# Kernel tuning notes

Hardware: AMD Instinct MI355X
Metric: run time of the kernel (lower is better)

Reference implementation:

```python
import jax, jax.numpy as jnp
import numpy as np

N_NODES = 100000


def gcn_conv(x, src, dst, W, b, n):
    # PyG GCNConv: h = x @ W; add self-loops; sym-normalize; scatter-add; + bias
    h = x @ W                                        # [N, out]
    loop = jnp.arange(n, dtype=src.dtype)
    src2 = jnp.concatenate([src, loop])              # [E+N]
    dst2 = jnp.concatenate([dst, loop])
    deg = jax.ops.segment_sum(jnp.ones_like(dst2, dtype=h.dtype), dst2, num_segments=n)
    dis = jnp.where(deg > 0, jax.lax.rsqrt(deg), 0.0)
    norm = dis[src2] * dis[dst2]                     # [E+N]
    msg = h[src2] * norm[:, None]                    # gather + scale
    out = jax.ops.segment_sum(msg, dst2, num_segments=n)  # scatter-add
    return out + b


def setup_inputs() -> dict:
    key = jax.random.key(0)
    ks = jax.random.split(key, 8)
    F_in, H = 128, 64
    E = 1200000
    x = jax.random.normal(ks[0], (N_NODES, F_in), dtype=jnp.float32)
    edge_index = jax.random.randint(ks[1], (2, E), 0, N_NODES, dtype=jnp.int64)
    s = 1.0 / np.sqrt(F_in)
    W1 = jax.random.normal(ks[2], (F_in, H), dtype=jnp.float32) * s
    b1 = jnp.zeros((H,), dtype=jnp.float32)
    W2 = jax.random.normal(ks[3], (H, H), dtype=jnp.float32) * (1.0 / np.sqrt(H))
    b2 = jnp.zeros((H,), dtype=jnp.float32)
    W3 = jax.random.normal(ks[4], (H, 1), dtype=jnp.float32) * (1.0 / np.sqrt(H))
    b3 = jnp.zeros((1,), dtype=jnp.float32)
    return {"x": x, "edge_index": edge_index, "W1": W1, "b1": b1,
            "W2": W2, "b2": b2, "W3": W3, "b3": b3}


def reference(x, edge_index, W1, b1, W2, b2, W3, b3):
    n = x.shape[0]
    src, dst = edge_index[0], edge_index[1]
    h = jax.nn.relu(gcn_conv(x, src, dst, W1, b1, n))
    h = jax.nn.relu(gcn_conv(h, src, dst, W2, b2, n))
    return (h @ W3 + b3)[:, 0]  # squeeze(-1) -> [N]
```

## Files before the change

kernel.cpp:

```cpp
#include <hip/hip_runtime.h>

#define NF 64
#define NBKMAX 512
#define CHUNK 4096
#define CAP   4096

typedef __attribute__((ext_vector_type(8))) short bf16x8;
typedef __attribute__((ext_vector_type(4))) float f32x4;

__device__ __forceinline__ unsigned short f2bf(float f) {
    union { float f; unsigned u; } c; c.f = f;
    unsigned u = c.u;
    return (unsigned short)((u + 0x7FFFu + ((u >> 16) & 1u)) >> 16);
}
__device__ __forceinline__ float bf2f1(unsigned short v) {
    union { unsigned u; float f; } c; c.u = ((unsigned)v) << 16;
    return c.f;
}
__device__ __forceinline__ float2 bfp2(unsigned v) {
    union { unsigned u; float f; } lo, hi;
    lo.u = v << 16;
    hi.u = v & 0xffff0000u;
    return make_float2(lo.f, hi.f);
}

__global__ void k_zero(int* __restrict__ p, int m) {
    int i = blockIdx.x * blockDim.x + threadIdx.x;
    if (i < m) p[i] = 0;
}

__global__ __launch_bounds__(256) void k_bscatter2(const int* __restrict__ src,
                                                   const int* __restrict__ dst,
                                                   int* __restrict__ bcnt,
                                                   uint2* __restrict__ pairs, int E, int nbk) {
    __shared__ int hist[NBKMAX];
    __shared__ int base[NBKMAX];
    __shared__ uint2 stage[CHUNK];
    int e0 = blockIdx.x * CHUNK;
    int cnt = E - e0; if (cnt > CHUNK) cnt = CHUNK;
    for (int i = threadIdx.x; i < nbk; i += 256) hist[i] = 0;
    __syncthreads();
    for (int i = threadIdx.x; i < cnt; i += 256) {
        int s = src[e0 + i], d = dst[e0 + i];
        stage[i] = make_uint2((unsigned)s, (unsigned)d);
        atomicAdd(&hist[((unsigned)d) >> 8], 1);
    }
    __syncthreads();
    for (int i = threadIdx.x; i < nbk; i += 256) {
        int c = hist[i];
        base[i] = c ? atomicAdd(&bcnt[i], c) : 0;
        hist[i] = 0;
    }
    __syncthreads();
    for (int i = threadIdx.x; i < cnt; i += 256) {
        uint2 p = stage[i];
        int b = p.y >> 8;
        int off = base[b] + atomicAdd(&hist[b], 1);
        if (off < CAP) pairs[(size_t)b * CAP + off] = p;
    }
}

__global__ __launch_bounds__(256) void k_bsort2(const uint2* __restrict__ pairs,
                                                const int* __restrict__ bcnt,
                                                int* __restrict__ start, int* __restrict__ endp,
                                                int* __restrict__ adj,
                                                float* __restrict__ dis, int n) {
    __shared__ int cnt[256];
    __shared__ int cur[256];
    int b   = blockIdx.x;
    int nb  = b << 8;
    int nn  = n - nb; if (nn > 256) nn = 256;
    int ec  = bcnt[b]; if (ec > CAP) ec = CAP;
    int pbI = b * CAP;
    size_t pb = (size_t)pbI;
    int t = threadIdx.x;
    cnt[t] = 0;
    __syncthreads();
    for (int i = t; i < ec; i += 256)
        atomicAdd(&cnt[pairs[pb + i].y & 255], 1);
    __syncthreads();
    int v = cnt[t];
    __syncthreads();
    for (int off = 1; off < 256; off <<= 1) {
        int u = (t >= off) ? cnt[t - off] : 0;
        __syncthreads();
        cnt[t] += u;
        __syncthreads();
    }
    int exc = cnt[t] - v;
    if (t < nn) {
        start[nb + t] = pbI + exc;
        endp[nb + t]  = pbI + exc + v;
        dis[nb + t]   = rsqrtf((float)(v + 1));
    }
    cur[t] = exc;
    __syncthreads();
    for (int i = t; i < ec; i += 256) {
        uint2 p = pairs[pb + i];
        int off = atomicAdd(&cur[p.y & 255], 1);
        adj[pbI + off] = (int)p.x;
    }
}

__global__ void k_wprep(const float* __restrict__ W, unsigned short* __restrict__ Wt_hi,
                        unsigned short* __restrict__ Wt_lo, int K) {
    int idx = blockIdx.x * 256 + threadIdx.x;
    if (idx >= K * 64) return;
    int k = idx >> 6, col = idx & 63;
    float w = W[idx];
    unsigned short h = f2bf(w);
    unsigned short l = f2bf(w - bf2f1(h));
    Wt_hi[col * K + k] = h;
    Wt_lo[col * K + k] = l;
}

__device__ __forceinline__ void load8f(const float* A, bool ok, size_t off, float* v) {
    if (ok) {
        float4 a = *(const float4*)&A[off];
        float4 b = *(const float4*)&A[off + 4];
        v[0]=a.x; v[1]=a.y; v[2]=a.z; v[3]=a.w;
        v[4]=b.x; v[5]=b.y; v[6]=b.z; v[7]=b.w;
    } else { for (int j = 0; j < 8; ++j) v[j] = 0.f; }
}
__device__ __forceinline__ void load8f(const unsigned short* A, bool ok, size_t off, float* v) {
    if (ok) {
        uint4 u = *(const uint4*)&A[off];
        float2 p0 = bfp2(u.x), p1 = bfp2(u.y), p2 = bfp2(u.z), p3 = bfp2(u.w);
        v[0]=p0.x; v[1]=p0.y; v[2]=p1.x; v[3]=p1.y;
        v[4]=p2.x; v[5]=p2.y; v[6]=p3.x; v[7]=p3.y;
    } else { for (int j = 0; j < 8; ++j) v[j] = 0.f; }
}

template<int K, typename AT>
__global__ __launch_bounds__(256) void k_mgemm(const AT* __restrict__ A,
                                               const unsigned short* __restrict__ Wt_hi_g,
                                               const unsigned short* __restrict__ Wt_lo_g,
                                               const float* __restrict__ bias_in,
                                               const float* __restrict__ dis,
                                               unsigned short* __restrict__ out, int n) {
    constexpr int KS = K / 8;
    constexpr int SM = KS - 1;
    __shared__ unsigned short sAh[64 * 32];
    __shared__ unsigned short sAl[64 * 32];
    __shared__ unsigned short sWh[64 * K];
    __shared__ unsigned short sWl[64 * K];
    const int tid = threadIdx.x;
    const int rb = blockIdx.x * 64;
    const int w  = tid >> 6, l = tid & 63;
    const int lr = l & 15, lg = l >> 4;
    const int srow = tid >> 2, skq = tid & 3;

    for (int idx = tid; idx < 64 * KS; idx += 256) {
        int col = idx / KS, slot = idx % KS;
        int d = col * K + 8 * (slot ^ (col & SM));
        *(uint4*)&sWh[d] = *(const uint4*)&Wt_hi_g[col * K + slot * 8];
        *(uint4*)&sWl[d] = *(const uint4*)&Wt_lo_g[col * K + slot * 8];
    }

    f32x4 acc[4] = {};

    for (int kb = 0; kb < K; kb += 32) {
        __syncthreads();
        {
            int rg = rb + srow;
            float v[8];
            load8f(A, rg < n, (size_t)rg * K + kb + skq * 8, v);
            if (bias_in) {
                #pragma unroll
                for (int j = 0; j < 8; ++j)
                    v[j] = fmaxf(v[j] + bias_in[kb + skq * 8 + j], 0.f);
            }
            unsigned short h8[8], l8[8];
            #pragma unroll
            for (int j = 0; j < 8; ++j) {
                h8[j] = f2bf(v[j]);
                l8[j] = f2bf(v[j] - bf2f1(h8[j]));
            }
            int d = srow * 32 + 8 * (skq ^ (srow & 3));
            *(uint4*)&sAh[d] = *(const uint4*)h8;
            *(uint4*)&sAl[d] = *(const uint4*)l8;
        }
        __syncthreads();

        int arow = w * 16 + lr;
        int aoff = arow * 32 + 8 * (lg ^ (arow & 3));
        const bf16x8 ah = *(const bf16x8*)&sAh[aoff];
        const bf16x8 al = *(const bf16x8*)&sAl[aoff];
        #pragma unroll
        for (int ct = 0; ct < 4; ++ct) {
            int col  = ct * 16 + lr;
            int boff = col * K + 8 * ((kb / 8 + lg) ^ (col & SM));
            const bf16x8 bh = *(const bf16x8*)&sWh[boff];
            const bf16x8 bl = *(const bf16x8*)&sWl[boff];
            acc[ct] = __builtin_amdgcn_mfma_f32_16x16x32_bf16(ah, bh, acc[ct], 0, 0, 0);
            acc[ct] = __builtin_amdgcn_mfma_f32_16x16x32_bf16(ah, bl, acc[ct], 0, 0, 0);
            acc[ct] = __builtin_amdgcn_mfma_f32_16x16x32_bf16(al, bh, acc[ct], 0, 0, 0);
        }
    }

    #pragma unroll
    for (int i = 0; i < 4; ++i) {
        int r = rb + w * 16 + lg * 4 + i;
        if (r < n) {
            float sc = dis[r];
            #pragma unroll
            for (int ct = 0; ct < 4; ++ct)
                out[(size_t)r * NF + ct * 16 + lr] = f2bf(acc[ct][i] * sc);
        }
    }
}

__global__ __launch_bounds__(256) void k_gather(const unsigned short* __restrict__ g,
                                                const int* __restrict__ adj,
                                                const int* __restrict__ start,
                                                const int* __restrict__ endp,
                                                const float* __restrict__ dis,
                                                unsigned short* __restrict__ agg, int n) {
    int node = blockIdx.x * 16 + (threadIdx.x >> 4);
    int fl   = threadIdx.x & 15;
    int gb   = threadIdx.x & 48;
    if (node >= n) return;
    int s = start[node], e = endp[node];
    uint2 v = *(const uint2*)&g[(size_t)node * NF + fl * 4];
    float2 pa = bfp2(v.x), pb = bfp2(v.y);
    float4 acc = make_float4(pa.x, pa.y, pb.x, pb.y);
    for (int base = s; base < e; base += 16) {
        int m = e - base; if (m > 16) m = 16;
        int idx = (fl < m) ? adj[base + fl] : 0;
        for (int j = 0; j < m; ++j) {
            int u = __shfl(idx, gb + j);
            uint2 w = *(const uint2*)&g[(size_t)u * NF + fl * 4];
            float2 q0 = bfp2(w.x), q1 = bfp2(w.y);
            acc.x += q0.x; acc.y += q0.y; acc.z += q1.x; acc.w += q1.y;
        }
    }
    float sc = dis[node];
    ushort4 o;
    o.x = f2bf(acc.x * sc);
    o.y = f2bf(acc.y * sc);
    o.z = f2bf(acc.z * sc);
    o.w = f2bf(acc.w * sc);
    *(ushort4*)&agg[(size_t)node * NF + fl * 4] = o;
}

__global__ __launch_bounds__(256) void k_gather_final(const unsigned short* __restrict__ g,
                                                      const int* __restrict__ adj,
                                                      const int* __restrict__ start,
                                                      const int* __restrict__ endp,
                                                      const float* __restrict__ dis,
                                                      const float* __restrict__ b2,
                                                      const float* __restrict__ W3,
                                                      const float* __restrict__ b3,
                                                      float* __restrict__ out, int n) {
    int node = blockIdx.x * 16 + (threadIdx.x >> 4);
    int fl   = threadIdx.x & 15;
    int gb   = threadIdx.x & 48;
    if (node >= n) return;
    int s = start[node], e = endp[node];
    uint2 v = *(const uint2*)&g[(size_t)node * NF + fl * 4];
    float2 pa = bfp2(v.x), pb = bfp2(v.y);
    float4 acc = make_float4(pa.x, pa.y, pb.x, pb.y);
    for (int base = s; base < e; base += 16) {
        int m = e - base; if (m > 16) m = 16;
        int idx = (fl < m) ? adj[base + fl] : 0;
        for (int j = 0; j < m; ++j) {
            int u = __shfl(idx, gb + j);
            uint2 w = *(const uint2*)&g[(size_t)u * NF + fl * 4];
            float2 q0 = bfp2(w.x), q1 = bfp2(w.y);
            acc.x += q0.x; acc.y += q0.y; acc.z += q1.x; acc.w += q1.y;
        }
    }
    float sc = dis[node];
    const float4 bb = *(const float4*)&b2[fl * 4];
    const float4 ww = *(const float4*)&W3[fl * 4];
    float r = fmaxf(acc.x * sc + bb.x, 0.f) * ww.x
            + fmaxf(acc.y * sc + bb.y, 0.f) * ww.y
            + fmaxf(acc.z * sc + bb.z, 0.f) * ww.z
            + fmaxf(acc.w * sc + bb.w, 0.f) * ww.w;
    #pragma unroll
    for (int off = 8; off > 0; off >>= 1) r += __shfl_down(r, off, 16);
    if (fl == 0) out[node] = r + b3[0];
}

extern "C" void kernel_launch(void* const* d_in, const int* in_sizes, int n_in,
                              void* d_out, int out_size, void* d_ws, size_t ws_size,
                              hipStream_t stream) {
    const float* x  = (const float*)d_in[0];
    const int*   ei = (const int*)d_in[1];
    const float* W1 = (const float*)d_in[2];
    const float* b1 = (const float*)d_in[3];
    const float* W2 = (const float*)d_in[4];
    const float* b2 = (const float*)d_in[5];
    const float* W3 = (const float*)d_in[6];
    const float* b3 = (const float*)d_in[7];
    float* out = (float*)d_out;

    const int n = out_size;
    const int E = in_sizes[1] / 2;
    const int* src = ei;
    const int* dst = ei + E;
    const int ns  = (n + 255) & ~255;
    const int nbk = (n + 255) >> 8;

    char* w = (char*)d_ws;
    float* dis   = (float*)w;  w += (size_t)ns * 4;
    int*   start = (int*)w;    w += (size_t)ns * 4;
    int*   endp  = (int*)w;    w += (size_t)ns * 4;
    int*   adj   = (int*)w;    w += (size_t)nbk * CAP * 4;
    int*   bcnt  = (int*)w;    w += NBKMAX * 4;
    unsigned short* wt1h = (unsigned short*)w;  w += 64 * 128 * 2;
    unsigned short* wt1l = (unsigned short*)w;  w += 64 * 128 * 2;
    unsigned short* wt2h = (unsigned short*)w;  w += 64 * 64 * 2;
    unsigned short* wt2l = (unsigned short*)w;  w += 64 * 64 * 2;
    unsigned short* gbuf1 = (unsigned short*)w;  w += (size_t)n * NF * 2;
    unsigned short* gbuf2 = (unsigned short*)w;  w += (size_t)n * NF * 2;
    unsigned short* aggb  = (unsigned short*)w;  w += (size_t)n * NF * 2;
    uint2* pairs = (uint2*)w;

    const int B = 256;

    k_zero<<<(nbk + B - 1) / B, B, 0, stream>>>(bcnt, nbk);
    k_wprep<<<(128 * 64 + B - 1) / B, B, 0, stream>>>(W1, wt1h, wt1l, 128);
    k_wprep<<<(64 * 64 + B - 1) / B, B, 0, stream>>>(W2, wt2h, wt2l, 64);
    k_bscatter2<<<(E + CHUNK - 1) / CHUNK, B, 0, stream>>>(src, dst, bcnt, pairs, E, nbk);
    k_bsort2<<<nbk, B, 0, stream>>>(pairs, bcnt, start, endp, adj, dis, n);

    k_mgemm<128, float><<<(n + 63) / 64, B, 0, stream>>>(x, wt1h, wt1l, nullptr, dis, gbuf1, n);
    k_gather<<<(n + 15) / 16, B, 0, stream>>>(gbuf1, adj, start, endp, dis, aggb, n);

    k_mgemm<64, unsigned short><<<(n + 63) / 64, B, 0, stream>>>(aggb, wt2h, wt2l, b1, dis, gbuf2, n);
    k_gather_final<<<(n + 15) / 16, B, 0, stream>>>(gbuf2, adj, start, endp, dis, b2, W3, b3, out, n);
}
```

Baseline: 140.1 us.

## Fuse edge bucketing with first GEMM and pack edge pairs into one word

Result: faster. 134.6 us (-3.9%).

```diff
diff --git a/kernel.cpp b/kernel.cpp
--- a/kernel.cpp
+++ b/kernel.cpp
@@ -24,43 +24,151 @@
     return make_float2(lo.f, hi.f);
 }
 
-__global__ void k_zero(int* __restrict__ p, int m) {
-    int i = blockIdx.x * blockDim.x + threadIdx.x;
-    if (i < m) p[i] = 0;
-}
-
-__global__ __launch_bounds__(256) void k_bscatter2(const int* __restrict__ src,
-                                                   const int* __restrict__ dst,
-                                                   int* __restrict__ bcnt,
-                                                   uint2* __restrict__ pairs, int E, int nbk) {
-    __shared__ int hist[NBKMAX];
-    __shared__ int base[NBKMAX];
-    __shared__ uint2 stage[CHUNK];
-    int e0 = blockIdx.x * CHUNK;
-    int cnt = E - e0; if (cnt > CHUNK) cnt = CHUNK;
-    for (int i = threadIdx.x; i < nbk; i += 256) hist[i] = 0;
-    __syncthreads();
-    for (int i = threadIdx.x; i < cnt; i += 256) {
-        int s = src[e0 + i], d = dst[e0 + i];
-        stage[i] = make_uint2((unsigned)s, (unsigned)d);
-        atomicAdd(&hist[((unsigned)d) >> 8], 1);
-    }
-    __syncthreads();
-    for (int i = threadIdx.x; i < nbk; i += 256) {
-        int c = hist[i];
-        base[i] = c ? atomicAdd(&bcnt[i], c) : 0;
-        hist[i] = 0;
-    }
-    __syncthreads();
-    for (int i = threadIdx.x; i < cnt; i += 256) {
-        uint2 p = stage[i];
-        int b = p.y >> 8;
-        int off = base[b] + atomicAdd(&hist[b], 1);
-        if (off < CAP) pairs[(size_t)b * CAP + off] = p;
-    }
-}
-
-__global__ __launch_bounds__(256) void k_bsort2(const uint2* __restrict__ pairs,
+__global__ __launch_bounds__(256) void k_prep(int* __restrict__ bcnt, int nbk,
+                                              const float* __restrict__ W1,
+                                              unsigned short* __restrict__ wt1h,
+                                              unsigned short* __restrict__ wt1l,
+                                              const float* __restrict__ W2,
+                                              unsigned short* __restrict__ wt2h,
+                                              unsigned short* __restrict__ wt2l) {
+    int idx = blockIdx.x * 256 + threadIdx.x;
+    if (idx < 512) {
+        if (idx < nbk) bcnt[idx] = 0;
+    } else if (idx < 512 + 128 * 64) {
+        int e = idx - 512;
+        int k = e >> 6, col = e & 63;
+        float w = W1[e];
+        unsigned short h = f2bf(w);
+        wt1h[col * 128 + k] = h;
+        wt1l[col * 128 + k] = f2bf(w - bf2f1(h));
+    } else if (idx < 512 + 128 * 64 + 64 * 64) {
+        int e = idx - 512 - 128 * 64;
+        int k = e >> 6, col = e & 63;
+        float w = W2[e];
+        unsigned short h = f2bf(w);
+        wt2h[col * 64 + k] = h;
+        wt2l[col * 64 + k] = f2bf(w - bf2f1(h));
+    }
+}
+
+struct ScatS {
+    unsigned stage[CHUNK];
+    unsigned short stb[CHUNK];
+    int hist[NBKMAX];
+    int base[NBKMAX];
+};
+struct GemmS {
+    unsigned short sAh[64 * 32];
+    unsigned short sAl[64 * 32];
+    unsigned short sWh[64 * 128];
+    unsigned short sWl[64 * 128];
+};
+union USmem { ScatS s; GemmS g; };
+
+__device__ __forceinline__ void load8f_f(const float* A, bool ok, size_t off, float* v) {
+    if (ok) {
+        float4 a = *(const float4*)&A[off];
+        float4 b = *(const float4*)&A[off + 4];
+        v[0]=a.x; v[1]=a.y; v[2]=a.z; v[3]=a.w;
+        v[4]=b.x; v[5]=b.y; v[6]=b.z; v[7]=b.w;
+    } else { for (int j = 0; j < 8; ++j) v[j] = 0.f; }
+}
+
+__global__ __launch_bounds__(256) void k_scat_gemm(
+        const int* __restrict__ src, const int* __restrict__ dst,
+        int* __restrict__ bcnt, unsigned* __restrict__ pairs4, int E, int nbk, int nscat,
+        const float* __restrict__ A,
+        const unsigned short* __restrict__ Wt_hi_g, const unsigned short* __restrict__ Wt_lo_g,
+        unsigned short* __restrict__ out, int n) {
+    __shared__ USmem u;
+    const int tid = threadIdx.x;
+
+    if ((int)blockIdx.x < nscat) {
+        int e0 = blockIdx.x * CHUNK;
+        int cnt = E - e0; if (cnt > CHUNK) cnt = CHUNK;
+        for (int i = tid; i < nbk; i += 256) u.s.hist[i] = 0;
+        __syncthreads();
+        for (int i = tid; i < cnt; i += 256) {
+            int s = src[e0 + i], d = dst[e0 + i];
+            u.s.stage[i] = ((unsigned)s << 8) | ((unsigned)d & 255u);
+            u.s.stb[i]   = (unsigned short)(((unsigned)d) >> 8);
+            atomicAdd(&u.s.hist[((unsigned)d) >> 8], 1);
+        }
+        __syncthreads();
+        for (int i = tid; i < nbk; i += 256) {
+            int c = u.s.hist[i];
+            u.s.base[i] = c ? atomicAdd(&bcnt[i], c) : 0;
+            u.s.hist[i] = 0;
+        }
+        __syncthreads();
+        for (int i = tid; i < cnt; i += 256) {
+            int b = u.s.stb[i];
+            int off = u.s.base[b] + atomicAdd(&u.s.hist[b], 1);
+            if (off < CAP) pairs4[(size_t)b * CAP + off] = u.s.stage[i];
+        }
+        return;
+    }
+
+    constexpr int K = 128;
+    constexpr int KS = K / 8, SM = KS - 1;
+    const int rb = ((int)blockIdx.x - nscat) * 64;
+    const int w  = tid >> 6, l = tid & 63;
+    const int lr = l & 15, lg = l >> 4;
+    const int srow = tid >> 2, skq = tid & 3;
+
+    for (int idx = tid; idx < 64 * KS; idx += 256) {
+        int col = idx / KS, slot = idx % KS;
+        int d = col * K + 8 * (slot ^ (col & SM));
+        *(uint4*)&u.g.sWh[d] = *(const uint4*)&Wt_hi_g[col * K + slot * 8];
+        *(uint4*)&u.g.sWl[d] = *(const uint4*)&Wt_lo_g[col * K + slot * 8];
+    }
+
+    f32x4 acc[4] = {};
+    for (int kb = 0; kb < K; kb += 32) {
+        __syncthreads();
+        {
+            int rg = rb + srow;
+            float v[8];
+            load8f_f(A, rg < n, (size_t)rg * K + kb + skq * 8, v);
+            unsigned short h8[8], l8[8];
+            #pragma unroll
+            for (int j = 0; j < 8; ++j) {
+                h8[j] = f2bf(v[j]);
+                l8[j] = f2bf(v[j] - bf2f1(h8[j]));
+            }
+            int d = srow * 32 + 8 * (skq ^ (srow & 3));
+            *(uint4*)&u.g.sAh[d] = *(const uint4*)h8;
+            *(uint4*)&u.g.sAl[d] = *(const uint4*)l8;
+        }
+        __syncthreads();
+
+        int arow = w * 16 + lr;
+        int aoff = arow * 32 + 8 * (lg ^ (arow & 3));
+        const bf16x8 ah = *(const bf16x8*)&u.g.sAh[aoff];
+        const bf16x8 al = *(const bf16x8*)&u.g.sAl[aoff];
+        #pragma unroll
+        for (int ct = 0; ct < 4; ++ct) {
+            int col  = ct * 16 + lr;
+            int boff = col * K + 8 * ((kb / 8 + lg) ^ (col & SM));
+            const bf16x8 bh = *(const bf16x8*)&u.g.sWh[boff];
+            const bf16x8 bl = *(const bf16x8*)&u.g.sWl[boff];
+            acc[ct] = __builtin_amdgcn_mfma_f32_16x16x32_bf16(ah, bh, acc[ct], 0, 0, 0);
+            acc[ct] = __builtin_amdgcn_mfma_f32_16x16x32_bf16(ah, bl, acc[ct], 0, 0, 0);
+            acc[ct] = __builtin_amdgcn_mfma_f32_16x16x32_bf16(al, bh, acc[ct], 0, 0, 0);
+        }
+    }
+    #pragma unroll
+    for (int i = 0; i < 4; ++i) {
+        int r = rb + w * 16 + lg * 4 + i;
+        if (r < n) {
+            #pragma unroll
+            for (int ct = 0; ct < 4; ++ct)
+                out[(size_t)r * NF + ct * 16 + lr] = f2bf(acc[ct][i]);
+        }
+    }
+}
+
+__global__ __launch_bounds__(256) void k_bsort2(const unsigned* __restrict__ pairs4,
                                                 const int* __restrict__ bcnt,
                                                 int* __restrict__ start, int* __restrict__ endp,
                                                 int* __restrict__ adj,
@@ -77,7 +185,7 @@
     cnt[t] = 0;
     __syncthreads();
     for (int i = t; i < ec; i += 256)
-        atomicAdd(&cnt[pairs[pb + i].y & 255], 1);
+        atomicAdd(&cnt[pairs4[pb + i] & 255u], 1);
     __syncthreads();
     int v = cnt[t];
     __syncthreads();
@@ -96,50 +204,19 @@
     cur[t] = exc;
     __syncthreads();
     for (int i = t; i < ec; i += 256) {
-        uint2 p = pairs[pb + i];
-        int off = atomicAdd(&cur[p.y & 255], 1);
-        adj[pbI + off] = (int)p.x;
-    }
-}
-
-__global__ void k_wprep(const float* __restrict__ W, unsigned short* __restrict__ Wt_hi,
-                        unsigned short* __restrict__ Wt_lo, int K) {
-    int idx = blockIdx.x * 256 + threadIdx.x;
-    if (idx >= K * 64) return;
-    int k = idx >> 6, col = idx & 63;
-    float w = W[idx];
-    unsigned short h = f2bf(w);
-    unsigned short l = f2bf(w - bf2f1(h));
-    Wt_hi[col * K + k] = h;
-    Wt_lo[col * K + k] = l;
-}
-
-__device__ __forceinline__ void load8f(const float* A, bool ok, size_t off, float* v) {
-    if (ok) {
-        float4 a = *(const float4*)&A[off];
-        float4 b = *(const float4*)&A[off + 4];
-        v[0]=a.x; v[1]=a.y; v[2]=a.z; v[3]=a.w;
-        v[4]=b.x; v[5]=b.y; v[6]=b.z; v[7]=b.w;
-    } else { for (int j = 0; j < 8; ++j) v[j] = 0.f; }
-}
-__device__ __forceinline__ void load8f(const unsigned short* A, bool ok, size_t off, float* v) {
-    if (ok) {
-        uint4 u = *(const uint4*)&A[off];
-        float2 p0 = bfp2(u.x), p1 = bfp2(u.y), p2 = bfp2(u.z), p3 = bfp2(u.w);
-        v[0]=p0.x; v[1]=p0.y; v[2]=p1.x; v[3]=p1.y;
-        v[4]=p2.x; v[5]=p2.y; v[6]=p3.x; v[7]=p3.y;
-    } else { for (int j = 0; j < 8; ++j) v[j] = 0.f; }
-}
-
-template<int K, typename AT>
-__global__ __launch_bounds__(256) void k_mgemm(const AT* __restrict__ A,
-                                               const unsigned short* __restrict__ Wt_hi_g,
-                                               const unsigned short* __restrict__ Wt_lo_g,
-                                               const float* __restrict__ bias_in,
-                                               const float* __restrict__ dis,
-                                               unsigned short* __restrict__ out, int n) {
-    constexpr int KS = K / 8;
-    constexpr int SM = KS - 1;
+        unsigned p = pairs4[pb + i];
+        int off = atomicAdd(&cur[p & 255u], 1);
+        adj[pbI + off] = (int)(p >> 8);
+    }
+}
+
+__global__ __launch_bounds__(256) void k_mgemm64(const unsigned short* __restrict__ A,
+                                                 const unsigned short* __restrict__ Wt_hi_g,
+                                                 const unsigned short* __restrict__ Wt_lo_g,
+                                                 const float* __restrict__ bias_in,
+                                                 unsigned short* __restrict__ out, int n) {
+    constexpr int K = 64;
+    constexpr int KS = K / 8, SM = KS - 1;
     __shared__ unsigned short sAh[64 * 32];
     __shared__ unsigned short sAl[64 * 32];
     __shared__ unsigned short sWh[64 * K];
@@ -158,18 +235,20 @@
     }
 
     f32x4 acc[4] = {};
-
     for (int kb = 0; kb < K; kb += 32) {
         __syncthreads();
         {
             int rg = rb + srow;
             float v[8];
-            load8f(A, rg < n, (size_t)rg * K + kb + skq * 8, v);
-            if (bias_in) {
-                #pragma unroll
-                for (int j = 0; j < 8; ++j)
-                    v[j] = fmaxf(v[j] + bias_in[kb + skq * 8 + j], 0.f);
-            }
+            if (rg < n) {
+                uint4 uu = *(const uint4*)&A[(size_t)rg * K + kb + skq * 8];
+                float2 p0 = bfp2(uu.x), p1 = bfp2(uu.y), p2 = bfp2(uu.z), p3 = bfp2(uu.w);
+                v[0]=p0.x; v[1]=p0.y; v[2]=p1.x; v[3]=p1.y;
+                v[4]=p2.x; v[5]=p2.y; v[6]=p3.x; v[7]=p3.y;
+            } else { for (int j = 0; j < 8; ++j) v[j] = 0.f; }
+            #pragma unroll
+            for (int j = 0; j < 8; ++j)
+                v[j] = fmaxf(v[j] + bias_in[kb + skq * 8 + j], 0.f);
             unsigned short h8[8], l8[8];
             #pragma unroll
             for (int j = 0; j < 8; ++j) {
@@ -197,15 +276,13 @@
             acc[ct] = __builtin_amdgcn_mfma_f32_16x16x32_bf16(al, bh, acc[ct], 0, 0, 0);
         }
     }
-
     #pragma unroll
     for (int i = 0; i < 4; ++i) {
         int r = rb + w * 16 + lg * 4 + i;
         if (r < n) {
-            float sc = dis[r];
             #pragma unroll
             for (int ct = 0; ct < 4; ++ct)
-                out[(size_t)r * NF + ct * 16 + lr] = f2bf(acc[ct][i] * sc);
+                out[(size_t)r * NF + ct * 16 + lr] = f2bf(acc[ct][i]);
         }
     }
 }
@@ -221,25 +298,27 @@
     int gb   = threadIdx.x & 48;
     if (node >= n) return;
     int s = start[node], e = endp[node];
+    float dn = dis[node];
     uint2 v = *(const uint2*)&g[(size_t)node * NF + fl * 4];
     float2 pa = bfp2(v.x), pb = bfp2(v.y);
-    float4 acc = make_float4(pa.x, pa.y, pb.x, pb.y);
+    float4 acc = make_float4(pa.x * dn, pa.y * dn, pb.x * dn, pb.y * dn);
     for (int base = s; base < e; base += 16) {
         int m = e - base; if (m > 16) m = 16;
         int idx = (fl < m) ? adj[base + fl] : 0;
         for (int j = 0; j < m; ++j) {
             int u = __shfl(idx, gb + j);
+            float du = dis[u];
             uint2 w = *(const uint2*)&g[(size_t)u * NF + fl * 4];
             float2 q0 = bfp2(w.x), q1 = bfp2(w.y);
-            acc.x += q0.x; acc.y += q0.y; acc.z += q1.x; acc.w += q1.y;
-        }
-    }
-    float sc = dis[node];
+            acc.x += q0.x * du; acc.y += q0.y * du;
+            acc.z += q1.x * du; acc.w += q1.y * du;
+        }
+    }
     ushort4 o;
-    o.x = f2bf(acc.x * sc);
-    o.y = f2bf(acc.y * sc);
-    o.z = f2bf(acc.z * sc);
-    o.w = f2bf(acc.w * sc);
+    o.x = f2bf(acc.x * dn);
+    o.y = f2bf(acc.y * dn);
+    o.z = f2bf(acc.z * dn);
+    o.w = f2bf(acc.w * dn);
     *(ushort4*)&agg[(size_t)node * NF + fl * 4] = o;
 }
 
@@ -257,26 +336,28 @@
     int gb   = threadIdx.x & 48;
     if (node >= n) return;
     int s = start[node], e = endp[node];
+    float dn = dis[node];
     uint2 v = *(const uint2*)&g[(size_t)node * NF + fl * 4];
     float2 pa = bfp2(v.x), pb = bfp2(v.y);
-    float4 acc = make_float4(pa.x, pa.y, pb.x, pb.y);
+    float4 acc = make_float4(pa.x * dn, pa.y * dn, pb.x * dn, pb.y * dn);
     for (int base = s; base < e; base += 16) {
         int m = e - base; if (m > 16) m = 16;
         int idx = (fl < m) ? adj[base + fl] : 0;
         for (int j = 0; j < m; ++j) {
             int u = __shfl(idx, gb + j);
+            float du = dis[u];
             uint2 w = *(const uint2*)&g[(size_t)u * NF + fl * 4];
             float2 q0 = bfp2(w.x), q1 = bfp2(w.y);
-            acc.x += q0.x; acc.y += q0.y; acc.z += q1.x; acc.w += q1.y;
-        }
-    }
-    float sc = dis[node];
+            acc.x += q0.x * du; acc.y += q0.y * du;
+            acc.z += q1.x * du; acc.w += q1.y * du;
+        }
+    }
     const float4 bb = *(const float4*)&b2[fl * 4];
     const float4 ww = *(const float4*)&W3[fl * 4];
-    float r = fmaxf(acc.x * sc + bb.x, 0.f) * ww.x
-            + fmaxf(acc.y * sc + bb.y, 0.f) * ww.y
-            + fmaxf(acc.z * sc + bb.z, 0.f) * ww.z
-            + fmaxf(acc.w * sc + bb.w, 0.f) * ww.w;
+    float r = fmaxf(acc.x * dn + bb.x, 0.f) * ww.x
+            + fmaxf(acc.y * dn + bb.y, 0.f) * ww.y
+            + fmaxf(acc.z * dn + bb.z, 0.f) * ww.z
+            + fmaxf(acc.w * dn + bb.w, 0.f) * ww.w;
     #pragma unroll
     for (int off = 8; off > 0; off >>= 1) r += __shfl_down(r, off, 16);
     if (fl == 0) out[node] = r + b3[0];
@@ -315,19 +396,20 @@
     unsigned short* gbuf1 = (unsigned short*)w;  w += (size_t)n * NF * 2;
     unsigned short* gbuf2 = (unsigned short*)w;  w += (size_t)n * NF * 2;
     unsigned short* aggb  = (unsigned short*)w;  w += (size_t)n * NF * 2;
-    uint2* pairs = (uint2*)w;
+    unsigned* pairs4 = (unsigned*)w;
 
     const int B = 256;
-
-    k_zero<<<(nbk + B - 1) / B, B, 0, stream>>>(bcnt, nbk);
-    k_wprep<<<(128 * 64 + B - 1) / B, B, 0, stream>>>(W1, wt1h, wt1l, 128);
-    k_wprep<<<(64 * 64 + B - 1) / B, B, 0, stream>>>(W2, wt2h, wt2l, 64);
-    k_bscatter2<<<(E + CHUNK - 1) / CHUNK, B, 0, stream>>>(src, dst, bcnt, pairs, E, nbk);
-    k_bsort2<<<nbk, B, 0, stream>>>(pairs, bcnt, start, endp, adj, dis, n);
-
-    k_mgemm<128, float><<<(n + 63) / 64, B, 0, stream>>>(x, wt1h, wt1l, nullptr, dis, gbuf1, n);
+    const int nscat = (E + CHUNK - 1) / CHUNK;
+    const int ngemm = (n + 63) / 64;
+
+    k_prep<<<(512 + 128 * 64 + 64 * 64 + B - 1) / B, B, 0, stream>>>(
+        bcnt, nbk, W1, wt1h, wt1l, W2, wt2h, wt2l);
+    k_scat_gemm<<<nscat + ngemm, B, 0, stream>>>(
+        src, dst, bcnt, pairs4, E, nbk, nscat, x, wt1h, wt1l, gbuf1, n);
+    k_bsort2<<<nbk, B, 0, stream>>>(pairs4, bcnt, start, endp, adj, dis, n);
+
     k_gather<<<(n + 15) / 16, B, 0, stream>>>(gbuf1, adj, start, endp, dis, aggb, n);
 
-    k_mgemm<64, unsigned short><<<(n + 63) / 64, B, 0, stream>>>(aggb, wt2h, wt2l, b1, dis, gbuf2, n);
+    k_mgemm64<<<ngemm, B, 0, stream>>>(aggb, wt2h, wt2l, b1, gbuf2, n);
     k_gather_final<<<(n + 15) / 16, B, 0, stream>>>(gbuf2, adj, start, endp, dis, b2, W3, b3, out, n);
 }
```
